# Kernel optimization log

Measured on AMD Instinct MI355X. Metric: run time of the kernel, lower is better.

Reference implementation:

```python
import jax, jax.numpy as jnp
import numpy as np

N = 8192
D_IN = 128
D_OUT = 128


def setup_inputs() -> dict:
    key = jax.random.key(0)
    k1, k2, k3, k4 = jax.random.split(key, 4)
    x = jax.random.normal(k1, (N, D_IN), dtype=jnp.float32)
    adj = jax.random.uniform(k2, (N, N), dtype=jnp.float32)
    # nn.Linear params: weight [out, in], bias [out]
    bound = 1.0 / np.sqrt(D_IN)
    W = jax.random.uniform(k3, (D_OUT, D_IN), minval=-bound, maxval=bound, dtype=jnp.float32)
    b = jax.random.uniform(k4, (D_OUT,), minval=-bound, maxval=bound, dtype=jnp.float32)
    return {"x": x, "adj": adj, "W": W, "b": b}


def reference(x, adj, W, b):
    # Symmetric normalization: D^{-1/2} A D^{-1/2}, expressed as fused
    # row/col scaling instead of materializing diagonal matrices.
    rowsum = adj.sum(axis=1)                      # [N]
    d_inv_sqrt = jnp.power(rowsum, -0.5)
    d_inv_sqrt = jnp.where(jnp.isinf(d_inv_sqrt), 0.0, d_inv_sqrt)
    adj_norm = d_inv_sqrt[:, None] * adj * d_inv_sqrt[None, :]  # [N, N]
    h = adj_norm @ x                              # [N, D_IN]
    return h @ W.T + b                            # [N, D_OUT]
```

## Files before the change

### kernel.cpp

```cpp
#include <hip/hip_runtime.h>
#include <hip/hip_bf16.h>

typedef short bf16x8 __attribute__((ext_vector_type(8)));
typedef float f32x16 __attribute__((ext_vector_type(16)));
typedef float f32x4v __attribute__((ext_vector_type(4)));

#define GN 8192
#define GD 128
#define KSPLIT 8


__global__ __launch_bounds__(256) void k_rowcvt(const float* __restrict__ adj,
                                                float* __restrict__ s,
                                                __hip_bfloat16* __restrict__ adjb) {
  const int row = blockIdx.x;
  const int t = threadIdx.x;
  const f32x4v* p = (const f32x4v*)(adj + (size_t)row * GN);
  f32x4v v[8];
  float acc = 0.f;
#pragma unroll
  for (int i = 0; i < 8; ++i) {
    v[i] = __builtin_nontemporal_load(p + t + i * 256);
    acc += (v[i].x + v[i].y) + (v[i].z + v[i].w);
  }
#pragma unroll
  for (int off = 32; off > 0; off >>= 1) acc += __shfl_down(acc, off, 64);
  __shared__ float red[4];
  __shared__ float sbc;
  if ((t & 63) == 0) red[t >> 6] = acc;
  __syncthreads();
  if (t == 0) {
    float tot = (red[0] + red[1]) + (red[2] + red[3]);
    float sc = (tot > 0.f) ? rsqrtf(tot) : 0.f;
    sbc = sc;
    s[row] = sc;
  }
  __syncthreads();
  const float sc = sbc;
  __hip_bfloat16* orow = adjb + (size_t)row * GN;
#pragma unroll
  for (int i = 0; i < 8; ++i) {
    __hip_bfloat16 hb[4];
    hb[0] = __float2bfloat16(v[i].x * sc);
    hb[1] = __float2bfloat16(v[i].y * sc);
    hb[2] = __float2bfloat16(v[i].z * sc);
    hb[3] = __float2bfloat16(v[i].w * sc);
    *(uint2*)(orow + (size_t)(t + i * 256) * 4) = *(uint2*)hb;
  }
}

__global__ __launch_bounds__(256) void k_pack(const float* __restrict__ x,
                                              const float* __restrict__ s,
                                              __hip_bfloat16* __restrict__ xsp) {
  const int kb = blockIdx.x;
  const int t = threadIdx.x;
  __shared__ float tile[64][129];
  __shared__ float sv[64];
  if (t < 64) sv[t] = s[kb * 64 + t];
  __syncthreads();
  const float4* xp = (const float4*)(x + (size_t)kb * 64 * GD);
#pragma unroll
  for (int j = 0; j < 8; ++j) {
    int i = t + j * 256;
    int r = i >> 5, c4 = i & 31;
    float4 v = xp[i];
    float sc = sv[r];
    tile[r][c4 * 4 + 0] = v.x * sc;
    tile[r][c4 * 4 + 1] = v.y * sc;
    tile[r][c4 * 4 + 2] = v.z * sc;
    tile[r][c4 * 4 + 3] = v.w * sc;
  }
  __syncthreads();
  const int c = t >> 1, h = t & 1;
  __hip_bfloat16 buf[32];
#pragma unroll
  for (int kk = 0; kk < 32; ++kk) buf[kk] = __float2bfloat16(tile[h * 32 + kk][c]);
  __hip_bfloat16* op = xsp + (size_t)kb * (128 * 72) + c * 72 + h * 32;
#pragma unroll
  for (int j = 0; j < 4; ++j) ((uint4*)op)[j] = ((uint4*)buf)[j];
}

__global__ __launch_bounds__(256, 4) void k_gemm(const __hip_bfloat16* __restrict__ adjb,
                                                 const __hip_bfloat16* __restrict__ xsp,
                                                 float* __restrict__ part) {
  __shared__ __align__(16) __hip_bfloat16 Asm[64 * 72];
  __shared__ __align__(16) __hip_bfloat16 Bsm[128 * 72];
  const int mb = blockIdx.x;
  const int ks = blockIdx.y;
  const int t = threadIdx.x;
  const int lane = t & 63;
  const int wave = t >> 6;
  const int wm = wave >> 1, wn = wave & 1;

  f32x16 acc0, acc1;
#pragma unroll
  for (int i = 0; i < 16; ++i) { acc0[i] = 0.f; acc1[i] = 0.f; }

  const int ar = t >> 2;
  const int acg = (t & 3) * 16;
  const __hip_bfloat16* arow = adjb + (size_t)(mb * 64 + ar) * GN + ks * 1024 + acg;
  const uint4* bsrc_base = (const uint4*)(xsp + (size_t)(ks * 16) * (128 * 72));

  const int a_lds_off = ar * 72 + acg;
  const int afrag_row = wm * 32 + (lane & 31);
  const int koff = (lane >> 5) * 8;
  const int bcol0 = wn * 64 + (lane & 31);

  for (int kt = 0; kt < 16; ++kt) {
    {
      const uint4* s4 = (const uint4*)(arow + (size_t)kt * 64);
      uint4 q0 = s4[0];
      uint4 q1 = s4[1];
      uint4* d = (uint4*)(Asm + a_lds_off);
      d[0] = q0;
      d[1] = q1;
    }
    {
      const uint4* bsv = bsrc_base + (size_t)kt * 1152;
      uint4* bd = (uint4*)Bsm;
      for (int i = t; i < 1152; i += 256) bd[i] = bsv[i];
    }
    __syncthreads();
#pragma unroll
    for (int kk = 0; kk < 64; kk += 16) {
      bf16x8 af = *(const bf16x8*)(Asm + afrag_row * 72 + kk + koff);
      bf16x8 b0 = *(const bf16x8*)(Bsm + bcol0 * 72 + kk + koff);
      bf16x8 b1 = *(const bf16x8*)(Bsm + (bcol0 + 32) * 72 + kk + koff);
      acc0 = __builtin_amdgcn_mfma_f32_32x32x16_bf16(af, b0, acc0, 0, 0, 0);
      acc1 = __builtin_amdgcn_mfma_f32_32x32x16_bf16(af, b1, acc1, 0, 0, 0);
    }
    __syncthreads();
  }

  float* pb = part + (size_t)ks * GN * GD + (size_t)(mb * 64 + wm * 32) * GD + wn * 64;
#pragma unroll
  for (int reg = 0; reg < 16; ++reg) {
    int r = (reg & 3) + 8 * (reg >> 2) + 4 * (lane >> 5);
    int cc = lane & 31;
    pb[(size_t)r * GD + cc] = acc0[reg];
    pb[(size_t)r * GD + cc + 32] = acc1[reg];
  }
}

__global__ __launch_bounds__(256) void k_out(const float* __restrict__ part,
                                             const float* __restrict__ W,
                                             const float* __restrict__ b,
                                             float* __restrict__ out) {
  __shared__ __align__(16) __hip_bfloat16 Hs[32 * 136];
  __shared__ __align__(16) __hip_bfloat16 Ws[128 * 136];
  __shared__ float bs[128];
  const int t = threadIdx.x;
  const int rowbase = blockIdx.x * 32;
  if (t < 128) bs[t] = b[t];
#pragma unroll
  for (int j = 0; j < 4; ++j) {
    int i = t + j * 256;
    int r = i >> 5, c4 = i & 31;
    size_t idx = (size_t)(rowbase + r) * GD + c4 * 4;
    float4 a = {0.f, 0.f, 0.f, 0.f};
#pragma unroll
    for (int ksl = 0; ksl < KSPLIT; ++ksl) {
      float4 p = *(const float4*)(part + idx + (size_t)ksl * GN * GD);
      a.x += p.x; a.y += p.y; a.z += p.z; a.w += p.w;
    }
    __hip_bfloat16 hb[4];
    hb[0] = __float2bfloat16(a.x);
    hb[1] = __float2bfloat16(a.y);
    hb[2] = __float2bfloat16(a.z);
    hb[3] = __float2bfloat16(a.w);
    *(uint2*)(Hs + r * 136 + c4 * 4) = *(uint2*)hb;
  }
#pragma unroll
  for (int j = 0; j < 16; ++j) {
    int i = t + j * 256;
    int o = i >> 5, k4 = i & 31;
    float4 w = *(const float4*)(W + (size_t)o * GD + k4 * 4);
    __hip_bfloat16 hb[4];
    hb[0] = __float2bfloat16(w.x);
    hb[1] = __float2bfloat16(w.y);
    hb[2] = __float2bfloat16(w.z);
    hb[3] = __float2bfloat16(w.w);
    *(uint2*)(Ws + o * 136 + k4 * 4) = *(uint2*)hb;
  }
  __syncthreads();
  const int lane = t & 63;
  const int wave = t >> 6;
  const int arow = lane & 31;
  const int koff = (lane >> 5) * 8;
  const int bcol = wave * 32 + (lane & 31);
  f32x16 acc;
#pragma unroll
  for (int i = 0; i < 16; ++i) acc[i] = 0.f;
#pragma unroll
  for (int kk = 0; kk < 128; kk += 16) {
    bf16x8 af = *(const bf16x8*)(Hs + arow * 136 + kk + koff);
    bf16x8 bf = *(const bf16x8*)(Ws + bcol * 136 + kk + koff);
    acc = __builtin_amdgcn_mfma_f32_32x32x16_bf16(af, bf, acc, 0, 0, 0);
  }
#pragma unroll
  for (int reg = 0; reg < 16; ++reg) {
    int r = (reg & 3) + 8 * (reg >> 2) + 4 * (lane >> 5);
    out[(size_t)(rowbase + r) * GD + bcol] = acc[reg] + bs[bcol];
  }
}

extern "C" void kernel_launch(void* const* d_in, const int* in_sizes, int n_in,
                              void* d_out, int out_size, void* d_ws, size_t ws_size,
                              hipStream_t stream) {
  const float* x   = (const float*)d_in[0];
  const float* adj = (const float*)d_in[1];
  const float* W   = (const float*)d_in[2];
  const float* b   = (const float*)d_in[3];
  float* out = (float*)d_out;

  float* s = (float*)d_ws;
  __hip_bfloat16* xsp  = (__hip_bfloat16*)((char*)d_ws + 32768);
  __hip_bfloat16* adjb = (__hip_bfloat16*)((char*)d_ws + 2392064);
  float* part = (float*)((char*)d_ws + 136609792);

  k_rowcvt<<<8192, 256, 0, stream>>>(adj, s, adjb);
  k_pack<<<128, 256, 0, stream>>>(x, s, xsp);
  k_gemm<<<dim3(128, KSPLIT), 256, 0, stream>>>(adjb, xsp, part);
  k_out<<<256, 256, 0, stream>>>(part, W, b, out);
}
```

Baseline: 414.1 us.

## Double GEMM M-tile to 128 rows and load B tile via global_load_lds

The adjacency GEMM block now covers 128 rows instead of 64, and each wave computes a 64x64 sub-tile with four MFMA accumulators, so every B (scaled x) tile loaded into LDS is reused twice as often. B tiles are now copied straight from global memory into LDS with the async global_load_lds builtin rather than through registers. The grid halves to 64x8 blocks (512 total), which may leave part of the 256 CUs idle or reduce latency hiding, and the higher register use lowers the occupancy hint to 2.

```diff
diff --git a/kernel.cpp b/kernel.cpp
--- a/kernel.cpp
+++ b/kernel.cpp
@@ -80,10 +80,10 @@
   for (int j = 0; j < 4; ++j) ((uint4*)op)[j] = ((uint4*)buf)[j];
 }
 
-__global__ __launch_bounds__(256, 4) void k_gemm(const __hip_bfloat16* __restrict__ adjb,
+__global__ __launch_bounds__(256, 2) void k_gemm(const __hip_bfloat16* __restrict__ adjb,
                                                  const __hip_bfloat16* __restrict__ xsp,
                                                  float* __restrict__ part) {
-  __shared__ __align__(16) __hip_bfloat16 Asm[64 * 72];
+  __shared__ __align__(16) __hip_bfloat16 Asm[128 * 72];
   __shared__ __align__(16) __hip_bfloat16 Bsm[128 * 72];
   const int mb = blockIdx.x;
   const int ks = blockIdx.y;
@@ -92,53 +92,66 @@
   const int wave = t >> 6;
   const int wm = wave >> 1, wn = wave & 1;
 
-  f32x16 acc0, acc1;
-#pragma unroll
-  for (int i = 0; i < 16; ++i) { acc0[i] = 0.f; acc1[i] = 0.f; }
-
-  const int ar = t >> 2;
-  const int acg = (t & 3) * 16;
-  const __hip_bfloat16* arow = adjb + (size_t)(mb * 64 + ar) * GN + ks * 1024 + acg;
-  const uint4* bsrc_base = (const uint4*)(xsp + (size_t)(ks * 16) * (128 * 72));
-
-  const int a_lds_off = ar * 72 + acg;
-  const int afrag_row = wm * 32 + (lane & 31);
+  f32x16 acc00, acc01, acc10, acc11;
+#pragma unroll
+  for (int i = 0; i < 16; ++i) {
+    acc00[i] = 0.f; acc01[i] = 0.f; acc10[i] = 0.f; acc11[i] = 0.f;
+  }
+
+  const int ar = t >> 1;
+  const int ah = (t & 1) * 32;
+  const __hip_bfloat16* arow = adjb + (size_t)(mb * 128 + ar) * GN + ks * 1024 + ah;
+  const char* bsrc_base = (const char*)(xsp + (size_t)(ks * 16) * (128 * 72));
+
+  const int a_lds_off = ar * 72 + ah;
+  const int afrag_row = wm * 64 + (lane & 31);
   const int koff = (lane >> 5) * 8;
   const int bcol0 = wn * 64 + (lane & 31);
 
   for (int kt = 0; kt < 16; ++kt) {
     {
+      const char* bg = bsrc_base + (size_t)kt * 18432;
+#pragma unroll
+      for (int c = 0; c < 5; ++c) {
+        int chunk = wave + c * 4;
+        if (chunk < 18) {
+          __builtin_amdgcn_global_load_lds(
+              (const __attribute__((address_space(1))) unsigned int*)(bg + chunk * 1024 + lane * 16),
+              (__attribute__((address_space(3))) unsigned int*)((char*)Bsm + chunk * 1024),
+              16, 0, 0);
+        }
+      }
+    }
+    {
       const uint4* s4 = (const uint4*)(arow + (size_t)kt * 64);
-      uint4 q0 = s4[0];
-      uint4 q1 = s4[1];
+      uint4 q0 = s4[0], q1 = s4[1], q2 = s4[2], q3 = s4[3];
       uint4* d = (uint4*)(Asm + a_lds_off);
-      d[0] = q0;
-      d[1] = q1;
-    }
-    {
-      const uint4* bsv = bsrc_base + (size_t)kt * 1152;
-      uint4* bd = (uint4*)Bsm;
-      for (int i = t; i < 1152; i += 256) bd[i] = bsv[i];
+      d[0] = q0; d[1] = q1; d[2] = q2; d[3] = q3;
     }
     __syncthreads();
 #pragma unroll
     for (int kk = 0; kk < 64; kk += 16) {
-      bf16x8 af = *(const bf16x8*)(Asm + afrag_row * 72 + kk + koff);
+      bf16x8 a0 = *(const bf16x8*)(Asm + afrag_row * 72 + kk + koff);
+      bf16x8 a1 = *(const bf16x8*)(Asm + (afrag_row + 32) * 72 + kk + koff);
       bf16x8 b0 = *(const bf16x8*)(Bsm + bcol0 * 72 + kk + koff);
       bf16x8 b1 = *(const bf16x8*)(Bsm + (bcol0 + 32) * 72 + kk + koff);
-      acc0 = __builtin_amdgcn_mfma_f32_32x32x16_bf16(af, b0, acc0, 0, 0, 0);
-      acc1 = __builtin_amdgcn_mfma_f32_32x32x16_bf16(af, b1, acc1, 0, 0, 0);
+      acc00 = __builtin_amdgcn_mfma_f32_32x32x16_bf16(a0, b0, acc00, 0, 0, 0);
+      acc01 = __builtin_amdgcn_mfma_f32_32x32x16_bf16(a0, b1, acc01, 0, 0, 0);
+      acc10 = __builtin_amdgcn_mfma_f32_32x32x16_bf16(a1, b0, acc10, 0, 0, 0);
+      acc11 = __builtin_amdgcn_mfma_f32_32x32x16_bf16(a1, b1, acc11, 0, 0, 0);
     }
     __syncthreads();
   }
 
-  float* pb = part + (size_t)ks * GN * GD + (size_t)(mb * 64 + wm * 32) * GD + wn * 64;
+  float* pb = part + (size_t)ks * GN * GD + (size_t)(mb * 128) * GD;
 #pragma unroll
   for (int reg = 0; reg < 16; ++reg) {
-    int r = (reg & 3) + 8 * (reg >> 2) + 4 * (lane >> 5);
-    int cc = lane & 31;
-    pb[(size_t)r * GD + cc] = acc0[reg];
-    pb[(size_t)r * GD + cc + 32] = acc1[reg];
+    int r0 = wm * 64 + (reg & 3) + 8 * (reg >> 2) + 4 * (lane >> 5);
+    int c0 = wn * 64 + (lane & 31);
+    pb[(size_t)r0 * GD + c0] = acc00[reg];
+    pb[(size_t)r0 * GD + c0 + 32] = acc01[reg];
+    pb[(size_t)(r0 + 32) * GD + c0] = acc10[reg];
+    pb[(size_t)(r0 + 32) * GD + c0 + 32] = acc11[reg];
   }
 }
 
@@ -220,6 +233,6 @@
 
   k_rowcvt<<<8192, 256, 0, stream>>>(adj, s, adjb);
   k_pack<<<128, 256, 0, stream>>>(x, s, xsp);
-  k_gemm<<<dim3(128, KSPLIT), 256, 0, stream>>>(adjb, xsp, part);
+  k_gemm<<<dim3(64, KSPLIT), 256, 0, stream>>>(adjb, xsp, part);
   k_out<<<256, 256, 0, stream>>>(part, W, b, out);
 }
```

After: 398.3 us. 3.8% less time.
